# Kernel optimization log

Measured on AMD Instinct MI355X. Metric: run time of the kernel, lower is better.

The kernel has to match this reference:

```python
import jax, jax.numpy as jnp
import numpy as np
from jax import lax

STRIDE = (1, 1)
PADDING = ((1, 1), (1, 1))  # stride=1, padding=1 for 3x3 conv


def setup_inputs() -> dict:
    key = jax.random.key(0)
    k1, k2 = jax.random.split(key)
    x = jax.random.normal(k1, (16, 32, 224, 224), dtype=jnp.float32)
    # kaiming_normal_(mode='fan_out', nonlinearity='relu'): std = sqrt(2/fan_out)
    fan_out = 32 * 3 * 3
    weight = jax.random.normal(k2, (32, 32, 3, 3), dtype=jnp.float32) * np.sqrt(2.0 / fan_out)
    return {"x": x, "weight": weight}


def reference(x, weight):
    # absmax 8-bit activation fake-quant
    x_scale = jnp.abs(x).max() + 1e-5
    x_q = jnp.round(jnp.clip(x * 127.0 / x_scale, -128.0, 127.0))
    # BitNet b1.58 ternary weight fake-quant
    w_scale = jnp.abs(weight).mean() + 1e-5
    w_q = jnp.clip(jnp.round(weight / w_scale), -1.0, 1.0)
    # straight-through estimator (no-op in pure forward, kept for fidelity)
    w_ste = weight + lax.stop_gradient(w_q * w_scale - weight)
    x_ste = x + lax.stop_gradient(x_q * (x_scale / 127.0) - x)
    out = lax.conv_general_dilated(
        x_ste, w_ste,
        window_strides=STRIDE,
        padding=PADDING,
        dimension_numbers=("NCHW", "OIHW", "NCHW"),
    )
    return out
```

## Files before the change

kernel.cpp:

```cpp
#include <hip/hip_runtime.h>


typedef __attribute__((ext_vector_type(8))) short short8;
typedef __attribute__((ext_vector_type(4))) float f32x4;

#define HW    224
#define NCH   32
#define PLANE (HW * HW)
#define TH 8
#define TW 32
#define NX4   (16 * NCH * PLANE / 4)

__device__ __forceinline__ int lds_h(int pix, int c) {
    int sw = (pix & 3) ^ ((pix >> 2) & 3);
    return pix * 32 + (c & 7) + ((((c >> 3) ^ sw) & 3) << 3);
}

__device__ __forceinline__ unsigned short q8(float v) {
    float q = rintf(fminf(127.f, fmaxf(-128.f, v)));
    return (unsigned short)(__float_as_uint(q) >> 16);
}


__global__ __launch_bounds__(256) void absmax_kernel(const float* __restrict__ x,
                                                     const float* __restrict__ w,
                                                     unsigned* __restrict__ slots,
                                                     float* __restrict__ scal,
                                                     unsigned short* __restrict__ wbuf)
{
    int tid = threadIdx.x;
    int lane = tid & 63, wv = tid >> 6;

    if (blockIdx.x == 0) {
        float s = 0.f;
        for (int i = tid; i < 9216; i += 256) s += fabsf(w[i]);
        #pragma unroll
        for (int off = 32; off > 0; off >>= 1) s += __shfl_xor(s, off);
        __shared__ float sm[4];
        __shared__ float s_ws;
        if (lane == 0) sm[wv] = s;
        __syncthreads();
        if (tid == 0) {
            float wscale = (sm[0] + sm[1] + sm[2] + sm[3]) / 9216.f + 1e-5f;
            scal[0] = wscale;
            s_ws = wscale;
        }
        __syncthreads();
        float wscale = s_ws;
        for (int o = tid; o < 9216; o += 256) {
            int frag = o >> 9, rem = o & 511;
            int l = rem >> 3, j = rem & 7;
            int tap = frag >> 1, kb = frag & 1;
            int kout = kb * 16 + (l & 15);
            int c = ((l >> 4) << 3) + j;
            int r = tap / 3, ss = tap % 3;
            float wv2 = w[((kout * 32 + c) * 3 + r) * 3 + ss];
            float q = fminf(1.f, fmaxf(-1.f, rintf(wv2 / wscale)));
            wbuf[o] = (unsigned short)(__float_as_uint(q) >> 16);
        }
        return;
    }

    const float4* x4 = (const float4*)x;
    float m = 0.f;
    for (int i = (blockIdx.x - 1) * 256 + tid; i < NX4; i += 2048 * 256) {
        float4 v = x4[i];
        m = fmaxf(m, fmaxf(fmaxf(fabsf(v.x), fabsf(v.y)),
                           fmaxf(fabsf(v.z), fabsf(v.w))));
    }
    #pragma unroll
    for (int off = 32; off > 0; off >>= 1)
        m = fmaxf(m, __shfl_xor(m, off));
    __shared__ float wm[4];
    if (lane == 0) wm[wv] = m;
    __syncthreads();
    if (tid == 0) {
        m = fmaxf(fmaxf(wm[0], wm[1]), fmaxf(wm[2], wm[3]));
        slots[blockIdx.x - 1] = __float_as_uint(m);
    }
}

__global__ __launch_bounds__(256, 5) void conv_kernel(const float* __restrict__ x,
                                                      const unsigned short* __restrict__ wbuf,
                                                      const unsigned* __restrict__ slots,
                                                      const float* __restrict__ scal,
                                                      float* __restrict__ out)
{
    __shared__ __align__(16) unsigned short xs[340 * 32];
    __shared__ float sred[4];

    int bid = (blockIdx.x & 7) * 392 + (blockIdx.x >> 3);
    int tw = bid % 7;
    int rest = bid / 7;
    int th = rest % 28;
    int n  = rest / 28;
    int h0 = th * TH, w0 = tw * TW;

    int tid = threadIdx.x;
    int lane = tid & 63, wv = tid >> 6;

    const float* xn = x + n * (NCH * PLANE);

    int slot = tid & 7;
    int c = tid >> 3;
    const float* tb = xn + c * PLANE + w0 + slot * 4;
    int pixb = 1 + slot * 4;

    uint4 s0 = ((const uint4*)slots)[tid];
    uint4 s1 = ((const uint4*)slots)[tid + 256];
    float wscale = scal[0];

    float hv[3];
    #pragma unroll
    for (int it = 0; it < 3; ++it) {
        int e = tid + it * 256;
        hv[it] = 0.f;
        if (e < 640) {
            int side = e & 1, cc = (e >> 1) & 31, hp = e >> 6;
            int gh = h0 - 1 + hp;
            int gw = side ? (w0 + TW) : (w0 - 1);
            int ghc = gh < 0 ? 0 : (gh > HW - 1 ? HW - 1 : gh);
            int gwc = gw < 0 ? 0 : (gw > HW - 1 ? HW - 1 : gw);
            hv[it] = xn[cc * PLANE + ghc * HW + gwc];
        }
    }
    float4 va[5], vb[5];
    #pragma unroll
    for (int i = 0; i < 5; ++i) {
        int gh = h0 - 1 + i;
        int ghc = gh < 0 ? 0 : (gh > HW - 1 ? HW - 1 : gh);
        va[i] = *(const float4*)(tb + ghc * HW);
    }
    #pragma unroll
    for (int i = 0; i < 5; ++i) {
        int gh = h0 + 4 + i;
        int ghc = gh > HW - 1 ? HW - 1 : gh;
        vb[i] = *(const float4*)(tb + ghc * HW);
    }

    float m2 = fmaxf(fmaxf(fmaxf(__uint_as_float(s0.x), __uint_as_float(s0.y)),
                           fmaxf(__uint_as_float(s0.z), __uint_as_float(s0.w))),
                     fmaxf(fmaxf(__uint_as_float(s1.x), __uint_as_float(s1.y)),
                           fmaxf(__uint_as_float(s1.z), __uint_as_float(s1.w))));
    #pragma unroll
    for (int off = 32; off > 0; off >>= 1)
        m2 = fmaxf(m2, __shfl_xor(m2, off));
    if (lane == 0) sred[wv] = m2;
    __syncthreads();
    float xmax = fmaxf(fmaxf(sred[0], sred[1]), fmaxf(sred[2], sred[3]));
    float xscale = xmax + 1e-5f;
    float inv = 127.f / xscale;
    float osc = (xscale / 127.f) * wscale;

    #pragma unroll
    for (int i = 0; i < 5; ++i) {
        int gh = h0 - 1 + i;
        float vs = ((unsigned)gh < (unsigned)HW) ? inv : 0.f;
        int p0 = i * 34 + pixb;
        xs[lds_h(p0 + 0, c)] = q8(va[i].x * vs);
        xs[lds_h(p0 + 1, c)] = q8(va[i].y * vs);
        xs[lds_h(p0 + 2, c)] = q8(va[i].z * vs);
        xs[lds_h(p0 + 3, c)] = q8(va[i].w * vs);
    }
    #pragma unroll
    for (int it = 0; it < 3; ++it) {
        int e = tid + it * 256;
        if (e < 640) {
            int side = e & 1, cc = (e >> 1) & 31, hp = e >> 6;
            int gh = h0 - 1 + hp;
            int gw = side ? (w0 + TW) : (w0 - 1);
            float vs = ((unsigned)gh < (unsigned)HW && (unsigned)gw < (unsigned)HW)
                           ? inv : 0.f;
            xs[lds_h(hp * 34 + (side ? 33 : 0), cc)] = q8(hv[it] * vs);
        }
    }
    #pragma unroll
    for (int i = 0; i < 5; ++i) {
        int gh = h0 + 4 + i;
        float vs = (gh < HW) ? inv : 0.f;
        int p0 = (5 + i) * 34 + pixb;
        xs[lds_h(p0 + 0, c)] = q8(vb[i].x * vs);
        xs[lds_h(p0 + 1, c)] = q8(vb[i].y * vs);
        xs[lds_h(p0 + 2, c)] = q8(vb[i].z * vs);
        xs[lds_h(p0 + 3, c)] = q8(vb[i].w * vs);
    }
    __syncthreads();

    int ln = lane & 15, cb = lane >> 4;
    f32x4 acc[2][2][2] = {};
    const short8* wfp = (const short8*)wbuf;
    short8 wa = wfp[lane];
    short8 wb = wfp[64 + lane];
    for (int tap = 0; tap < 9; ++tap) {
        short8 na, nb;
        if (tap < 8) {
            na = wfp[(2 * tap + 2) * 64 + lane];
            nb = wfp[(2 * tap + 3) * 64 + lane];
        }
        int r = tap / 3;
        int s2 = tap - r * 3;
        #pragma unroll
        for (int ri = 0; ri < 2; ++ri) {
            #pragma unroll
            for (int pb = 0; pb < 2; ++pb) {
                int pix = (wv * 2 + ri + r) * 34 + pb * 16 + ln + s2;
                int sw = (pix & 3) ^ ((pix >> 2) & 3);
                const short8 a = *(const short8*)&xs[pix * 32 + (((cb ^ sw) & 3) << 3)];
                acc[ri][pb][0] = __builtin_amdgcn_mfma_f32_16x16x32_bf16(
                    a, wa, acc[ri][pb][0], 0, 0, 0);
                acc[ri][pb][1] = __builtin_amdgcn_mfma_f32_16x16x32_bf16(
                    a, wb, acc[ri][pb][1], 0, 0, 0);
            }
        }
        wa = na;
        wb = nb;
    }

    float* on = out + n * (NCH * PLANE);
    #pragma unroll
    for (int ri = 0; ri < 2; ++ri) {
        int h = h0 + wv * 2 + ri;
        #pragma unroll
        for (int pb = 0; pb < 2; ++pb) {
            int wcol = w0 + pb * 16 + cb * 4;
            #pragma unroll
            for (int kb = 0; kb < 2; ++kb) {
                int k = kb * 16 + ln;
                f32x4 o;
                o[0] = acc[ri][pb][kb][0] * osc;
                o[1] = acc[ri][pb][kb][1] * osc;
                o[2] = acc[ri][pb][kb][2] * osc;
                o[3] = acc[ri][pb][kb][3] * osc;
                *(f32x4*)&on[(k * HW + h) * HW + wcol] = o;
            }
        }
    }
}

extern "C" void kernel_launch(void* const* d_in, const int* in_sizes, int n_in,
                              void* d_out, int out_size, void* d_ws, size_t ws_size,
                              hipStream_t stream)
{
    const float* x = (const float*)d_in[0];
    const float* w = (const float*)d_in[1];
    float* outp = (float*)d_out;
    unsigned* slots = (unsigned*)d_ws;
    float* scal = (float*)((char*)d_ws + 8192);
    unsigned short* wbuf = (unsigned short*)((char*)d_ws + 8448);

    absmax_kernel<<<2049, 256, 0, stream>>>(x, w, slots, scal, wbuf);
    conv_kernel<<<16 * 28 * 7, 256, 0, stream>>>(x, wbuf, slots, scal, outp);
}
```

Before: 72.98 us.

## Make conv blocks persistent over four row tiles with prefetch and LDS weights

Each conv block now handles four consecutive 8-row tiles (32 rows) instead of one, with a quarter as many blocks launched. Weights are staged once into LDS, and the next tile's input rows are loaded into registers while the current tile's MFMAs run, so global load latency overlaps compute and the halo/slot/weight setup is amortized. The cost is more LDS per block, occupancy hint lowered from 5 to 4, only 784 blocks for the whole GPU, and an extra barrier per tile.

```diff
diff --git a/kernel.cpp b/kernel.cpp
--- a/kernel.cpp
+++ b/kernel.cpp
@@ -80,26 +80,29 @@
     }
 }
 
-__global__ __launch_bounds__(256, 5) void conv_kernel(const float* __restrict__ x,
+__global__ __launch_bounds__(256, 4) void conv_kernel(const float* __restrict__ x,
                                                       const unsigned short* __restrict__ wbuf,
                                                       const unsigned* __restrict__ slots,
                                                       const float* __restrict__ scal,
                                                       float* __restrict__ out)
 {
     __shared__ __align__(16) unsigned short xs[340 * 32];
+    __shared__ __align__(16) unsigned short wl[18 * 512];
     __shared__ float sred[4];
 
-    int bid = (blockIdx.x & 7) * 392 + (blockIdx.x >> 3);
+    int bid = (blockIdx.x & 7) * 98 + (blockIdx.x >> 3);
     int tw = bid % 7;
     int rest = bid / 7;
-    int th = rest % 28;
-    int n  = rest / 28;
-    int h0 = th * TH, w0 = tw * TW;
+    int qh = rest % 7;
+    int n  = rest / 7;
+    int w0 = tw * TW;
+    int hb = qh * 32;
 
     int tid = threadIdx.x;
     int lane = tid & 63, wv = tid >> 6;
 
     const float* xn = x + n * (NCH * PLANE);
+    float* on = out + n * (NCH * PLANE);
 
     int slot = tid & 7;
     int c = tid >> 3;
@@ -110,32 +113,42 @@
     uint4 s1 = ((const uint4*)slots)[tid + 256];
     float wscale = scal[0];
 
-    float hv[3];
-    #pragma unroll
-    for (int it = 0; it < 3; ++it) {
-        int e = tid + it * 256;
-        hv[it] = 0.f;
-        if (e < 640) {
-            int side = e & 1, cc = (e >> 1) & 31, hp = e >> 6;
-            int gh = h0 - 1 + hp;
-            int gw = side ? (w0 + TW) : (w0 - 1);
-            int ghc = gh < 0 ? 0 : (gh > HW - 1 ? HW - 1 : gh);
-            int gwc = gw < 0 ? 0 : (gw > HW - 1 ? HW - 1 : gw);
-            hv[it] = xn[cc * PLANE + ghc * HW + gwc];
-        }
-    }
-    float4 va[5], vb[5];
+    const short8* wfp = (const short8*)wbuf;
+    short8* wl8 = (short8*)wl;
     #pragma unroll
     for (int i = 0; i < 5; ++i) {
-        int gh = h0 - 1 + i;
-        int ghc = gh < 0 ? 0 : (gh > HW - 1 ? HW - 1 : gh);
-        va[i] = *(const float4*)(tb + ghc * HW);
-    }
-    #pragma unroll
-    for (int i = 0; i < 5; ++i) {
-        int gh = h0 + 4 + i;
-        int ghc = gh > HW - 1 ? HW - 1 : gh;
-        vb[i] = *(const float4*)(tb + ghc * HW);
+        int idx = tid + i * 256;
+        if (idx < 1152) wl8[idx] = wfp[idx];
+    }
+
+    float4 va[5], vb[5];
+    float hv[3];
+    {
+        int h0 = hb;
+        #pragma unroll
+        for (int i = 0; i < 5; ++i) {
+            int gh = h0 - 1 + i;
+            int ghc = gh < 0 ? 0 : gh;
+            va[i] = *(const float4*)(tb + ghc * HW);
+        }
+        #pragma unroll
+        for (int i = 0; i < 5; ++i) {
+            int gh = h0 + 4 + i;
+            vb[i] = *(const float4*)(tb + gh * HW);
+        }
+        #pragma unroll
+        for (int it = 0; it < 3; ++it) {
+            int e = tid + it * 256;
+            hv[it] = 0.f;
+            if (e < 640) {
+                int side = e & 1, cc = (e >> 1) & 31, hp = e >> 6;
+                int gh = h0 - 1 + hp;
+                int gw = side ? (w0 + TW) : (w0 - 1);
+                int ghc = gh < 0 ? 0 : gh;
+                int gwc = gw < 0 ? 0 : (gw > HW - 1 ? HW - 1 : gw);
+                hv[it] = xn[cc * PLANE + ghc * HW + gwc];
+            }
+        }
     }
 
     float m2 = fmaxf(fmaxf(fmaxf(__uint_as_float(s0.x), __uint_as_float(s0.y)),
@@ -152,88 +165,113 @@
     float inv = 127.f / xscale;
     float osc = (xscale / 127.f) * wscale;
 
-    #pragma unroll
-    for (int i = 0; i < 5; ++i) {
-        int gh = h0 - 1 + i;
-        float vs = ((unsigned)gh < (unsigned)HW) ? inv : 0.f;
-        int p0 = i * 34 + pixb;
-        xs[lds_h(p0 + 0, c)] = q8(va[i].x * vs);
-        xs[lds_h(p0 + 1, c)] = q8(va[i].y * vs);
-        xs[lds_h(p0 + 2, c)] = q8(va[i].z * vs);
-        xs[lds_h(p0 + 3, c)] = q8(va[i].w * vs);
-    }
-    #pragma unroll
-    for (int it = 0; it < 3; ++it) {
-        int e = tid + it * 256;
-        if (e < 640) {
-            int side = e & 1, cc = (e >> 1) & 31, hp = e >> 6;
-            int gh = h0 - 1 + hp;
-            int gw = side ? (w0 + TW) : (w0 - 1);
-            float vs = ((unsigned)gh < (unsigned)HW && (unsigned)gw < (unsigned)HW)
-                           ? inv : 0.f;
-            xs[lds_h(hp * 34 + (side ? 33 : 0), cc)] = q8(hv[it] * vs);
-        }
-    }
-    #pragma unroll
-    for (int i = 0; i < 5; ++i) {
-        int gh = h0 + 4 + i;
-        float vs = (gh < HW) ? inv : 0.f;
-        int p0 = (5 + i) * 34 + pixb;
-        xs[lds_h(p0 + 0, c)] = q8(vb[i].x * vs);
-        xs[lds_h(p0 + 1, c)] = q8(vb[i].y * vs);
-        xs[lds_h(p0 + 2, c)] = q8(vb[i].z * vs);
-        xs[lds_h(p0 + 3, c)] = q8(vb[i].w * vs);
-    }
-    __syncthreads();
-
     int ln = lane & 15, cb = lane >> 4;
-    f32x4 acc[2][2][2] = {};
-    const short8* wfp = (const short8*)wbuf;
-    short8 wa = wfp[lane];
-    short8 wb = wfp[64 + lane];
-    for (int tap = 0; tap < 9; ++tap) {
-        short8 na, nb;
-        if (tap < 8) {
-            na = wfp[(2 * tap + 2) * 64 + lane];
-            nb = wfp[(2 * tap + 3) * 64 + lane];
-        }
-        int r = tap / 3;
-        int s2 = tap - r * 3;
+
+    for (int t = 0; t < 4; ++t) {
+        int h0 = hb + t * TH;
+
+        #pragma unroll
+        for (int i = 0; i < 5; ++i) {
+            int gh = h0 - 1 + i;
+            float vs = ((unsigned)gh < (unsigned)HW) ? inv : 0.f;
+            int p0 = i * 34 + pixb;
+            xs[lds_h(p0 + 0, c)] = q8(va[i].x * vs);
+            xs[lds_h(p0 + 1, c)] = q8(va[i].y * vs);
+            xs[lds_h(p0 + 2, c)] = q8(va[i].z * vs);
+            xs[lds_h(p0 + 3, c)] = q8(va[i].w * vs);
+        }
+        #pragma unroll
+        for (int it = 0; it < 3; ++it) {
+            int e = tid + it * 256;
+            if (e < 640) {
+                int side = e & 1, cc = (e >> 1) & 31, hp = e >> 6;
+                int gh = h0 - 1 + hp;
+                int gw = side ? (w0 + TW) : (w0 - 1);
+                float vs = ((unsigned)gh < (unsigned)HW && (unsigned)gw < (unsigned)HW)
+                               ? inv : 0.f;
+                xs[lds_h(hp * 34 + (side ? 33 : 0), cc)] = q8(hv[it] * vs);
+            }
+        }
+        #pragma unroll
+        for (int i = 0; i < 5; ++i) {
+            int gh = h0 + 4 + i;
+            float vs = (gh < HW) ? inv : 0.f;
+            int p0 = (5 + i) * 34 + pixb;
+            xs[lds_h(p0 + 0, c)] = q8(vb[i].x * vs);
+            xs[lds_h(p0 + 1, c)] = q8(vb[i].y * vs);
+            xs[lds_h(p0 + 2, c)] = q8(vb[i].z * vs);
+            xs[lds_h(p0 + 3, c)] = q8(vb[i].w * vs);
+        }
+        __syncthreads();
+
+        if (t < 3) {
+            int h1 = h0 + TH;
+            #pragma unroll
+            for (int i = 0; i < 5; ++i) {
+                int gh = h1 - 1 + i;
+                va[i] = *(const float4*)(tb + gh * HW);
+            }
+            #pragma unroll
+            for (int i = 0; i < 5; ++i) {
+                int gh = h1 + 4 + i;
+                int ghc = gh > HW - 1 ? HW - 1 : gh;
+                vb[i] = *(const float4*)(tb + ghc * HW);
+            }
+            #pragma unroll
+            for (int it = 0; it < 3; ++it) {
+                int e = tid + it * 256;
+                if (e < 640) {
+                    int side = e & 1, cc = (e >> 1) & 31, hp = e >> 6;
+                    int gh = h1 - 1 + hp;
+                    int gw = side ? (w0 + TW) : (w0 - 1);
+                    int ghc = gh > HW - 1 ? HW - 1 : gh;
+                    int gwc = gw < 0 ? 0 : (gw > HW - 1 ? HW - 1 : gw);
+                    hv[it] = xn[cc * PLANE + ghc * HW + gwc];
+                }
+            }
+        }
+
+        f32x4 acc[2][2][2] = {};
+        #pragma unroll
+        for (int tap = 0; tap < 9; ++tap) {
+            short8 wa = wl8[(2 * tap) * 64 + lane];
+            short8 wb = wl8[(2 * tap + 1) * 64 + lane];
+            int r = tap / 3;
+            int s2 = tap - r * 3;
+            #pragma unroll
+            for (int ri = 0; ri < 2; ++ri) {
+                #pragma unroll
+                for (int pb = 0; pb < 2; ++pb) {
+                    int pix = (wv * 2 + ri + r) * 34 + pb * 16 + ln + s2;
+                    int sw = (pix & 3) ^ ((pix >> 2) & 3);
+                    const short8 a = *(const short8*)&xs[pix * 32 + (((cb ^ sw) & 3) << 3)];
+                    acc[ri][pb][0] = __builtin_amdgcn_mfma_f32_16x16x32_bf16(
+                        a, wa, acc[ri][pb][0], 0, 0, 0);
+                    acc[ri][pb][1] = __builtin_amdgcn_mfma_f32_16x16x32_bf16(
+                        a, wb, acc[ri][pb][1], 0, 0, 0);
+                }
+            }
+        }
+
         #pragma unroll
         for (int ri = 0; ri < 2; ++ri) {
+            int h = h0 + wv * 2 + ri;
             #pragma unroll
             for (int pb = 0; pb < 2; ++pb) {
-                int pix = (wv * 2 + ri + r) * 34 + pb * 16 + ln + s2;
-                int sw = (pix & 3) ^ ((pix >> 2) & 3);
-                const short8 a = *(const short8*)&xs[pix * 32 + (((cb ^ sw) & 3) << 3)];
-                acc[ri][pb][0] = __builtin_amdgcn_mfma_f32_16x16x32_bf16(
-                    a, wa, acc[ri][pb][0], 0, 0, 0);
-                acc[ri][pb][1] = __builtin_amdgcn_mfma_f32_16x16x32_bf16(
-                    a, wb, acc[ri][pb][1], 0, 0, 0);
-            }
-        }
-        wa = na;
-        wb = nb;
-    }
-
-    float* on = out + n * (NCH * PLANE);
-    #pragma unroll
-    for (int ri = 0; ri < 2; ++ri) {
-        int h = h0 + wv * 2 + ri;
-        #pragma unroll
-        for (int pb = 0; pb < 2; ++pb) {
-            int wcol = w0 + pb * 16 + cb * 4;
-            #pragma unroll
-            for (int kb = 0; kb < 2; ++kb) {
-                int k = kb * 16 + ln;
-                f32x4 o;
-                o[0] = acc[ri][pb][kb][0] * osc;
-                o[1] = acc[ri][pb][kb][1] * osc;
-                o[2] = acc[ri][pb][kb][2] * osc;
-                o[3] = acc[ri][pb][kb][3] * osc;
-                *(f32x4*)&on[(k * HW + h) * HW + wcol] = o;
-            }
-        }
+                int wcol = w0 + pb * 16 + cb * 4;
+                #pragma unroll
+                for (int kb = 0; kb < 2; ++kb) {
+                    int k = kb * 16 + ln;
+                    f32x4 o;
+                    o[0] = acc[ri][pb][kb][0] * osc;
+                    o[1] = acc[ri][pb][kb][1] * osc;
+                    o[2] = acc[ri][pb][kb][2] * osc;
+                    o[3] = acc[ri][pb][kb][3] * osc;
+                    *(f32x4*)&on[(k * HW + h) * HW + wcol] = o;
+                }
+            }
+        }
+        __syncthreads();
     }
 }
 
@@ -249,5 +287,5 @@
     unsigned short* wbuf = (unsigned short*)((char*)d_ws + 8448);
 
     absmax_kernel<<<2049, 256, 0, stream>>>(x, w, slots, scal, wbuf);
-    conv_kernel<<<16 * 28 * 7, 256, 0, stream>>>(x, wbuf, slots, scal, outp);
-}
+    conv_kernel<<<16 * 7 * 7, 256, 0, stream>>>(x, wbuf, slots, scal, outp);
+}
```

Measured after the change: 128.3 us. 1.76x slower.

## Move input tile loads after scale reduction and drop occupancy hint

Applied to the files above, without the earlier changes.

Input tile and halo loads no longer sit in registers before the absmax reduction barrier. They now run after the barrier in a loop unrolled by 2, with quantization applied right after each load. The launch_bounds minimum-blocks hint of 5 is removed. The change cuts live registers, but the tile loads no longer overlap with the slot reduction and sync, and the compiler may now pick a different register budget.

```diff
diff --git a/kernel.cpp b/kernel.cpp
--- a/kernel.cpp
+++ b/kernel.cpp
@@ -80,11 +80,11 @@
     }
 }
 
-__global__ __launch_bounds__(256, 5) void conv_kernel(const float* __restrict__ x,
-                                                      const unsigned short* __restrict__ wbuf,
-                                                      const unsigned* __restrict__ slots,
-                                                      const float* __restrict__ scal,
-                                                      float* __restrict__ out)
+__global__ __launch_bounds__(256) void conv_kernel(const float* __restrict__ x,
+                                                   const unsigned short* __restrict__ wbuf,
+                                                   const unsigned* __restrict__ slots,
+                                                   const float* __restrict__ scal,
+                                                   float* __restrict__ out)
 {
     __shared__ __align__(16) unsigned short xs[340 * 32];
     __shared__ float sred[4];
@@ -101,43 +101,9 @@
 
     const float* xn = x + n * (NCH * PLANE);
 
-    int slot = tid & 7;
-    int c = tid >> 3;
-    const float* tb = xn + c * PLANE + w0 + slot * 4;
-    int pixb = 1 + slot * 4;
-
     uint4 s0 = ((const uint4*)slots)[tid];
     uint4 s1 = ((const uint4*)slots)[tid + 256];
     float wscale = scal[0];
-
-    float hv[3];
-    #pragma unroll
-    for (int it = 0; it < 3; ++it) {
-        int e = tid + it * 256;
-        hv[it] = 0.f;
-        if (e < 640) {
-            int side = e & 1, cc = (e >> 1) & 31, hp = e >> 6;
-            int gh = h0 - 1 + hp;
-            int gw = side ? (w0 + TW) : (w0 - 1);
-            int ghc = gh < 0 ? 0 : (gh > HW - 1 ? HW - 1 : gh);
-            int gwc = gw < 0 ? 0 : (gw > HW - 1 ? HW - 1 : gw);
-            hv[it] = xn[cc * PLANE + ghc * HW + gwc];
-        }
-    }
-    float4 va[5], vb[5];
-    #pragma unroll
-    for (int i = 0; i < 5; ++i) {
-        int gh = h0 - 1 + i;
-        int ghc = gh < 0 ? 0 : (gh > HW - 1 ? HW - 1 : gh);
-        va[i] = *(const float4*)(tb + ghc * HW);
-    }
-    #pragma unroll
-    for (int i = 0; i < 5; ++i) {
-        int gh = h0 + 4 + i;
-        int ghc = gh > HW - 1 ? HW - 1 : gh;
-        vb[i] = *(const float4*)(tb + ghc * HW);
-    }
-
     float m2 = fmaxf(fmaxf(fmaxf(__uint_as_float(s0.x), __uint_as_float(s0.y)),
                            fmaxf(__uint_as_float(s0.z), __uint_as_float(s0.w))),
                      fmaxf(fmaxf(__uint_as_float(s1.x), __uint_as_float(s1.y)),
@@ -152,15 +118,23 @@
     float inv = 127.f / xscale;
     float osc = (xscale / 127.f) * wscale;
 
-    #pragma unroll
-    for (int i = 0; i < 5; ++i) {
-        int gh = h0 - 1 + i;
-        float vs = ((unsigned)gh < (unsigned)HW) ? inv : 0.f;
-        int p0 = i * 34 + pixb;
-        xs[lds_h(p0 + 0, c)] = q8(va[i].x * vs);
-        xs[lds_h(p0 + 1, c)] = q8(va[i].y * vs);
-        xs[lds_h(p0 + 2, c)] = q8(va[i].z * vs);
-        xs[lds_h(p0 + 3, c)] = q8(va[i].w * vs);
+    {
+        int slot = tid & 7;
+        int c = tid >> 3;
+        const float* tb = xn + c * PLANE + w0 + slot * 4;
+        int pixb = 1 + slot * 4;
+        #pragma unroll 2
+        for (int hp = 0; hp < 10; ++hp) {
+            int gh = h0 - 1 + hp;
+            int ghc = gh < 0 ? 0 : (gh > HW - 1 ? HW - 1 : gh);
+            float4 v = *(const float4*)(tb + ghc * HW);
+            float vs = (gh == ghc) ? inv : 0.f;
+            int p0 = hp * 34 + pixb;
+            xs[lds_h(p0 + 0, c)] = q8(v.x * vs);
+            xs[lds_h(p0 + 1, c)] = q8(v.y * vs);
+            xs[lds_h(p0 + 2, c)] = q8(v.z * vs);
+            xs[lds_h(p0 + 3, c)] = q8(v.w * vs);
+        }
     }
     #pragma unroll
     for (int it = 0; it < 3; ++it) {
@@ -169,20 +143,12 @@
             int side = e & 1, cc = (e >> 1) & 31, hp = e >> 6;
             int gh = h0 - 1 + hp;
             int gw = side ? (w0 + TW) : (w0 - 1);
-            float vs = ((unsigned)gh < (unsigned)HW && (unsigned)gw < (unsigned)HW)
-                           ? inv : 0.f;
-            xs[lds_h(hp * 34 + (side ? 33 : 0), cc)] = q8(hv[it] * vs);
-        }
-    }
-    #pragma unroll
-    for (int i = 0; i < 5; ++i) {
-        int gh = h0 + 4 + i;
-        float vs = (gh < HW) ? inv : 0.f;
-        int p0 = (5 + i) * 34 + pixb;
-        xs[lds_h(p0 + 0, c)] = q8(vb[i].x * vs);
-        xs[lds_h(p0 + 1, c)] = q8(vb[i].y * vs);
-        xs[lds_h(p0 + 2, c)] = q8(vb[i].z * vs);
-        xs[lds_h(p0 + 3, c)] = q8(vb[i].w * vs);
+            int ghc = gh < 0 ? 0 : (gh > HW - 1 ? HW - 1 : gh);
+            int gwc = gw < 0 ? 0 : (gw > HW - 1 ? HW - 1 : gw);
+            float v = xn[cc * PLANE + ghc * HW + gwc];
+            float vs = (gh == ghc && gw == gwc) ? inv : 0.f;
+            xs[lds_h(hp * 34 + (side ? 33 : 0), cc)] = q8(v * vs);
+        }
     }
     __syncthreads();
 
```

New measurement: 83.73 us. 1.15x slower.
